# Optimization experiments

Hardware: AMD Instinct MI355X
Metric: run time of the kernel (lower is better)

## Reference

```python
import jax, jax.numpy as jnp
import numpy as np

N = 50000
E = 400000
IN_DIM = 64
HID = 64
HEADS = 4
LN_EPS = 1e-5


def _glorot(key, shape):
    fan_in, fan_out = shape[-1], shape[0] if len(shape) > 1 else shape[-1]
    lim = jnp.sqrt(6.0 / (fan_in + fan_out))
    return jax.random.uniform(key, shape, jnp.float32, -lim, lim)


def setup_inputs() -> dict:
    key = jax.random.key(0)
    ks = jax.random.split(key, 24)
    x = jax.random.normal(ks[0], (N, IN_DIM), jnp.float32)
    edge_index = jax.random.randint(ks[1], (2, E), 0, N, jnp.int64)
    role_ids = jax.random.randint(ks[2], (N,), 0, 2, jnp.int64)
    # GAT layer 1: in IN_DIM -> HEADS*HID, concat
    W1 = _glorot(ks[3], (HEADS * HID, IN_DIM))
    a1s = _glorot(ks[4], (HEADS, HID))
    a1d = _glorot(ks[5], (HEADS, HID))
    b1 = jnp.zeros((HEADS * HID,), jnp.float32)
    # GAT layer 2: HEADS*HID -> HEADS*HID, concat
    W2 = _glorot(ks[6], (HEADS * HID, HEADS * HID))
    a2s = _glorot(ks[7], (HEADS, HID))
    a2d = _glorot(ks[8], (HEADS, HID))
    b2 = jnp.zeros((HEADS * HID,), jnp.float32)
    # GAT layer 3: HEADS*HID -> HID, 1 head, no concat
    W3 = _glorot(ks[9], (HID, HEADS * HID))
    a3s = _glorot(ks[10], (1, HID))
    a3d = _glorot(ks[11], (1, HID))
    b3 = jnp.zeros((HID,), jnp.float32)
    ln1_w = jnp.ones((HEADS * HID,), jnp.float32); ln1_b = jnp.zeros((HEADS * HID,), jnp.float32)
    ln2_w = jnp.ones((HEADS * HID,), jnp.float32); ln2_b = jnp.zeros((HEADS * HID,), jnp.float32)
    ln3_w = jnp.ones((HID,), jnp.float32); ln3_b = jnp.zeros((HID,), jnp.float32)
    role_table = jax.random.normal(ks[12], (2, HID), jnp.float32)
    p1_w = _glorot(ks[13], (HID, 2 * HID)); p1_b = jnp.zeros((HID,), jnp.float32)
    p2_w = _glorot(ks[14], (HID, HID)); p2_b = jnp.zeros((HID,), jnp.float32)
    return dict(x=x, edge_index=edge_index, role_ids=role_ids,
                W1=W1, a1s=a1s, a1d=a1d, b1=b1,
                W2=W2, a2s=a2s, a2d=a2d, b2=b2,
                W3=W3, a3s=a3s, a3d=a3d, b3=b3,
                ln1_w=ln1_w, ln1_b=ln1_b, ln2_w=ln2_w, ln2_b=ln2_b,
                ln3_w=ln3_w, ln3_b=ln3_b,
                role_table=role_table, p1_w=p1_w, p1_b=p1_b, p2_w=p2_w, p2_b=p2_b)


def gat_conv(x, src, dst, W, a_src, a_dst, bias, heads, out_ch, concat):
    # x: [N, F_in]; src/dst: [E'] (self loops already appended)
    n = x.shape[0]
    h = (x @ W.T).reshape(n, heads, out_ch)              # [N,H,C]
    score_s = jnp.einsum('nhc,hc->nh', h, a_src)          # [N,H]
    score_d = jnp.einsum('nhc,hc->nh', h, a_dst)
    e = jax.nn.leaky_relu(score_s[src] + score_d[dst], 0.2)   # [E,H]
    m = jax.ops.segment_max(e, dst, num_segments=n)       # per-dst softmax
    e = jnp.exp(e - m[dst])
    s = jax.ops.segment_sum(e, dst, num_segments=n)
    alpha = e / (s[dst] + 1e-16)                          # [E,H]
    msg = h[src] * alpha[:, :, None]                      # [E,H,C]
    out = jax.ops.segment_sum(msg, dst, num_segments=n)   # [N,H,C]
    out = out.reshape(n, heads * out_ch) if concat else out.mean(axis=1)
    return out + bias


def layer_norm(x, w, b):
    mu = jnp.mean(x, axis=-1, keepdims=True)
    var = jnp.mean(jnp.square(x - mu), axis=-1, keepdims=True)
    return (x - mu) * jax.lax.rsqrt(var + LN_EPS) * w + b


def reference(x, edge_index, role_ids, W1, a1s, a1d, b1, W2, a2s, a2d, b2,
              W3, a3s, a3d, b3, ln1_w, ln1_b, ln2_w, ln2_b, ln3_w, ln3_b,
              role_table, p1_w, p1_b, p2_w, p2_b):
    n = x.shape[0]
    loop = jnp.arange(n, dtype=edge_index.dtype)
    src = jnp.concatenate([edge_index[0], loop])
    dst = jnp.concatenate([edge_index[1], loop])
    h = jax.nn.elu(gat_conv(x, src, dst, W1, a1s, a1d, b1, HEADS, HID, True))
    h = layer_norm(h, ln1_w, ln1_b)
    h = jax.nn.elu(gat_conv(h, src, dst, W2, a2s, a2d, b2, HEADS, HID, True))
    h = layer_norm(h, ln2_w, ln2_b)
    h = gat_conv(h, src, dst, W3, a3s, a3d, b3, 1, HID, False)
    h = layer_norm(h, ln3_w, ln3_b)
    role_emb = role_table[role_ids]                        # [N,HID]
    z = jnp.concatenate([h, role_emb], axis=-1)            # [N,2*HID]
    z = jax.nn.relu(z @ p1_w.T + p1_b)
    z = z @ p2_w.T + p2_b
    return z
```

## Files before the change

### kernel.cpp

```cpp
#include <hip/hip_runtime.h>
#include <math.h>


using short8 = __attribute__((ext_vector_type(8))) short;
using f32x4  = __attribute__((ext_vector_type(4))) float;

#define LOG2E 1.44269504088896340736f

__device__ __forceinline__ unsigned short f2bf(float f) {
    unsigned int u = __builtin_bit_cast(unsigned int, f);
    u += 0x7fffu + ((u >> 16) & 1u);
    return (unsigned short)(u >> 16);
}
__device__ __forceinline__ float bflo(unsigned int w) {
    return __builtin_bit_cast(float, w << 16);
}
__device__ __forceinline__ float bfhi(unsigned int w) {
    return __builtin_bit_cast(float, w & 0xffff0000u);
}
__device__ __forceinline__ float fexp2(float x) {
    return __builtin_amdgcn_exp2f(x);
}

__global__ void k_f2bf(const float* __restrict__ in, unsigned short* __restrict__ out,
                       int n) {
    int i = (blockIdx.x * 256 + threadIdx.x) * 4;
    if (i >= n) return;
    float4 v = *reinterpret_cast<const float4*>(in + i);
    ushort4 u;
    u.x = f2bf(v.x); u.y = f2bf(v.y); u.z = f2bf(v.z); u.w = f2bf(v.w);
    *reinterpret_cast<ushort4*>(out + i) = u;
}

__global__ void k_f2bf_w(const float* __restrict__ s0, unsigned short* __restrict__ d0, int n0,
                         const float* __restrict__ s1, unsigned short* __restrict__ d1, int n1,
                         const float* __restrict__ s2, unsigned short* __restrict__ d2, int n2,
                         const float* __restrict__ s3, unsigned short* __restrict__ d3, int n3,
                         const float* __restrict__ s4, unsigned short* __restrict__ d4, int n4) {
    int i = (blockIdx.x * 256 + threadIdx.x) * 4;
    const float* s; unsigned short* d; int off = i;
    if (off < n0) { s = s0; d = d0; }
    else if ((off -= n0) < n1) { s = s1; d = d1; }
    else if ((off -= n1) < n2) { s = s2; d = d2; }
    else if ((off -= n2) < n3) { s = s3; d = d3; }
    else if ((off -= n3) < n4) { s = s4; d = d4; }
    else return;
    float4 v = *reinterpret_cast<const float4*>(s + off);
    ushort4 u;
    u.x = f2bf(v.x); u.y = f2bf(v.y); u.z = f2bf(v.z); u.w = f2bf(v.w);
    *reinterpret_cast<ushort4*>(d + off) = u;
}

__global__ void k_count(const int* __restrict__ ei, int* __restrict__ deg,
                        int N, int E, int E2) {
    int i = blockIdx.x * 256 + threadIdx.x;
    if (i >= E2) return;
    int d = (i < E) ? ei[E + i] : (i - E);
    atomicAdd(&deg[d], 1);
}

__device__ __forceinline__ int blk_scan_incl(int v, int tid) {
    int lane = tid & 63, w = tid >> 6;
#pragma unroll
    for (int off = 1; off < 64; off <<= 1) {
        int u = __shfl_up(v, off);
        if (lane >= off) v += u;
    }
    __shared__ int wsum[4];
    if (lane == 63) wsum[w] = v;
    __syncthreads();
    int add = 0;
#pragma unroll
    for (int k = 0; k < 4; ++k)
        if (k < w) add += wsum[k];
    return v + add;
}

__global__ __launch_bounds__(256) void k_bsum(const int* __restrict__ deg,
                                              int* __restrict__ bsum, int N) {
    int i = blockIdx.x * 256 + threadIdx.x;
    int v = (i < N) ? deg[i] : 0;
#pragma unroll
    for (int off = 32; off; off >>= 1) v += __shfl_down(v, off);
    __shared__ int ws[4];
    if ((threadIdx.x & 63) == 0) ws[threadIdx.x >> 6] = v;
    __syncthreads();
    if (threadIdx.x == 0) bsum[blockIdx.x] = ws[0] + ws[1] + ws[2] + ws[3];
}

__global__ __launch_bounds__(256) void k_bscan(const int* __restrict__ bsum,
                                               int* __restrict__ boff, int nb) {
    int t = threadIdx.x;
    int v = (t < nb) ? bsum[t] : 0;
    int incl = blk_scan_incl(v, t);
    if (t < nb) boff[t] = incl - v;
}

__global__ __launch_bounds__(256) void k_scatter(const int* __restrict__ deg,
                                                 const int* __restrict__ boff,
                                                 int* __restrict__ row_ptr,
                                                 int* __restrict__ cursor,
                                                 int N, int E2) {
    int tid = threadIdx.x;
    int i = blockIdx.x * 256 + tid;
    int d = (i < N) ? deg[i] : 0;
    int incl = blk_scan_incl(d, tid);
    int ex = incl - d + boff[blockIdx.x];
    if (i < N) { row_ptr[i] = ex; cursor[i] = ex; }
    if (i == 0) row_ptr[N] = E2;
}

__global__ void k_fill(const int* __restrict__ ei, int* __restrict__ cursor,
                       int* __restrict__ edge_src, int N, int E, int E2) {
    int i = blockIdx.x * 256 + threadIdx.x;
    if (i >= E2) return;
    int s_, d_;
    if (i < E) { s_ = ei[i]; d_ = ei[E + i]; }
    else       { s_ = d_ = i - E; }
    int pos = atomicAdd(&cursor[d_], 1);
    edge_src[pos] = s_;
}

template <int K, bool RELU, bool BF16OUT, bool SCORES>
__global__ __launch_bounds__(256) void k_gmfma(const unsigned short* __restrict__ A,
                                               const unsigned short* __restrict__ Wb,
                                               const float* __restrict__ bias,
                                               void* __restrict__ Cv,
                                               float* __restrict__ sS,
                                               float* __restrict__ sD,
                                               const float* __restrict__ a_s,
                                               const float* __restrict__ a_d,
                                               int M, int NC, int Hs) {
    constexpr int NSTEP = K / 32;
    __shared__ unsigned short As[2][64 * 32];
    __shared__ unsigned short Bs[2][64 * 32];
    int tid = threadIdx.x;
    int lane = tid & 63, wid = tid >> 6;
    int wm = wid & 1, wn = wid >> 1;
    int fr = lane & 15, fq = lane >> 4;
    int bm = blockIdx.x * 64, bn = blockIdx.y * 64;

    int lrow = lane >> 2, lkq = (lane & 3) * 8;

    auto stage = [&](int buf, int k0) {
        int ra = wid * 16;
        int arow = min(bm + ra + lrow, M - 1);
        __builtin_amdgcn_global_load_lds(
            (const __attribute__((address_space(1))) unsigned int*)
                (A + (size_t)arow * K + k0 + lkq),
            (__attribute__((address_space(3))) unsigned int*)&As[buf][ra * 32],
            16, 0, 0);
        __builtin_amdgcn_global_load_lds(
            (const __attribute__((address_space(1))) unsigned int*)
                (Wb + (size_t)(bn + ra + lrow) * K + k0 + lkq),
            (__attribute__((address_space(3))) unsigned int*)&Bs[buf][ra * 32],
            16, 0, 0);
    };

    f32x4 acc[2][2];
#pragma unroll
    for (int mt = 0; mt < 2; ++mt)
#pragma unroll
        for (int nt = 0; nt < 2; ++nt) acc[mt][nt] = f32x4{0.f, 0.f, 0.f, 0.f};

    stage(0, 0);
    __syncthreads();
    int cur = 0;
    for (int t = 0; t < NSTEP; ++t) {
        if (t + 1 < NSTEP) stage(cur ^ 1, (t + 1) * 32);
        short8 af[2], bfr[2];
#pragma unroll
        for (int mt = 0; mt < 2; ++mt)
            af[mt] = *reinterpret_cast<const short8*>(
                &As[cur][(wm * 32 + mt * 16 + fr) * 32 + fq * 8]);
#pragma unroll
        for (int nt = 0; nt < 2; ++nt)
            bfr[nt] = *reinterpret_cast<const short8*>(
                &Bs[cur][(wn * 32 + nt * 16 + fr) * 32 + fq * 8]);
#pragma unroll
        for (int mt = 0; mt < 2; ++mt)
#pragma unroll
            for (int nt = 0; nt < 2; ++nt)
                acc[mt][nt] = __builtin_amdgcn_mfma_f32_16x16x32_bf16(
                    af[mt], bfr[nt], acc[mt][nt], 0, 0, 0);
        __syncthreads();
        cur ^= 1;
    }

#pragma unroll
    for (int nt = 0; nt < 2; ++nt) {
        int col = bn + wn * 32 + nt * 16 + fr;
        float bv = bias ? bias[col] : 0.f;
#pragma unroll
        for (int mt = 0; mt < 2; ++mt) {
#pragma unroll
            for (int j = 0; j < 4; ++j) {
                int row = bm + wm * 32 + mt * 16 + fq * 4 + j;
                if (row < M) {
                    float v = acc[mt][nt][j] + bv;
                    if (RELU) v = fmaxf(v, 0.f);
                    if constexpr (BF16OUT)
                        ((unsigned short*)Cv)[(size_t)row * NC + col] = f2bf(v);
                    else
                        ((float*)Cv)[(size_t)row * NC + col] = v;
                }
            }
        }
    }

    if constexpr (SCORES) {
        __shared__ float sps[2][64];
        __shared__ float spd[2][64];
        int head = blockIdx.y;
        float as_c[2], ad_c[2];
#pragma unroll
        for (int nt = 0; nt < 2; ++nt) {
            int cw = wn * 32 + nt * 16 + fr;
            as_c[nt] = a_s[head * 64 + cw];
            ad_c[nt] = a_d[head * 64 + cw];
        }
#pragma unroll
        for (int mt = 0; mt < 2; ++mt) {
#pragma unroll
            for (int j = 0; j < 4; ++j) {
                float ps = acc[mt][0][j] * as_c[0] + acc[mt][1][j] * as_c[1];
                float pd = acc[mt][0][j] * ad_c[0] + acc[mt][1][j] * ad_c[1];
#pragma unroll
                for (int off = 1; off < 16; off <<= 1) {
                    ps += __shfl_xor(ps, off);
                    pd += __shfl_xor(pd, off);
                }
                if (fr == 0) {
                    int rl = wm * 32 + mt * 16 + fq * 4 + j;
                    sps[wn][rl] = ps;
                    spd[wn][rl] = pd;
                }
            }
        }
        __syncthreads();
        if (tid < 64) {
            int row = bm + tid;
            if (row < M) {
                sS[(size_t)row * Hs + head] = (sps[0][tid] + sps[1][tid]) * LOG2E;
                sD[(size_t)row * Hs + head] = (spd[0][tid] + spd[1][tid]) * LOG2E;
            }
        }
    }
}

__global__ __launch_bounds__(256) void k_mlp(const unsigned short* __restrict__ catb,
                                             const unsigned short* __restrict__ p1wb,
                                             const float* __restrict__ p1b,
                                             const unsigned short* __restrict__ p2wb,
                                             const float* __restrict__ p2b,
                                             float* __restrict__ outp, int M) {
    __shared__ unsigned short As[2][64 * 32];
    __shared__ unsigned short Z1[64 * 72];
    int tid = threadIdx.x;
    int lane = tid & 63, wid = tid >> 6;
    int wm = wid & 1, wn = wid >> 1;
    int fr = lane & 15, fq = lane >> 4;
    int bm = blockIdx.x * 64;
    int lrow = lane >> 2, lkq = (lane & 3) * 8;

    auto stageA = [&](int buf, int k0) {
        int ra = wid * 16;
        int arow = min(bm + ra + lrow, M - 1);
        __builtin_amdgcn_global_load_lds(
            (const __attribute__((address_space(1))) unsigned int*)
                (catb + (size_t)arow * 128 + k0 + lkq),
            (__attribute__((address_space(3))) unsigned int*)&As[buf][ra * 32],
            16, 0, 0);
    };

    f32x4 acc[2][2];
#pragma unroll
    for (int mt = 0; mt < 2; ++mt)
#pragma unroll
        for (int nt = 0; nt < 2; ++nt) acc[mt][nt] = f32x4{0.f, 0.f, 0.f, 0.f};
    stageA(0, 0);
    __syncthreads();
    int cur = 0;
    for (int t = 0; t < 4; ++t) {
        if (t + 1 < 4) stageA(cur ^ 1, (t + 1) * 32);
        short8 af[2], bfr[2];
#pragma unroll
        for (int mt = 0; mt < 2; ++mt)
            af[mt] = *reinterpret_cast<const short8*>(
                &As[cur][(wm * 32 + mt * 16 + fr) * 32 + fq * 8]);
#pragma unroll
        for (int nt = 0; nt < 2; ++nt)
            bfr[nt] = *reinterpret_cast<const short8*>(
                p1wb + (size_t)(wn * 32 + nt * 16 + fr) * 128 + t * 32 + fq * 8);
#pragma unroll
        for (int mt = 0; mt < 2; ++mt)
#pragma unroll
            for (int nt = 0; nt < 2; ++nt)
                acc[mt][nt] = __builtin_amdgcn_mfma_f32_16x16x32_bf16(
                    af[mt], bfr[nt], acc[mt][nt], 0, 0, 0);
        __syncthreads();
        cur ^= 1;
    }
#pragma unroll
    for (int nt = 0; nt < 2; ++nt) {
        int col = wn * 32 + nt * 16 + fr;
        float bv = p1b[col];
#pragma unroll
        for (int mt = 0; mt < 2; ++mt) {
#pragma unroll
            for (int j = 0; j < 4; ++j) {
                int rl = wm * 32 + mt * 16 + fq * 4 + j;
                Z1[rl * 72 + col] = f2bf(fmaxf(acc[mt][nt][j] + bv, 0.f));
            }
        }
    }
    __syncthreads();

    f32x4 acc2[2][2];
#pragma unroll
    for (int mt = 0; mt < 2; ++mt)
#pragma unroll
        for (int nt = 0; nt < 2; ++nt) acc2[mt][nt] = f32x4{0.f, 0.f, 0.f, 0.f};
#pragma unroll
    for (int t = 0; t < 2; ++t) {
        short8 af[2], bfr[2];
#pragma unroll
        for (int mt = 0; mt < 2; ++mt)
            af[mt] = *reinterpret_cast<const short8*>(
                &Z1[(wm * 32 + mt * 16 + fr) * 72 + t * 32 + fq * 8]);
#pragma unroll
        for (int nt = 0; nt < 2; ++nt)
            bfr[nt] = *reinterpret_cast<const short8*>(
                p2wb + (size_t)(wn * 32 + nt * 16 + fr) * 64 + t * 32 + fq * 8);
#pragma unroll
        for (int mt = 0; mt < 2; ++mt)
#pragma unroll
            for (int nt = 0; nt < 2; ++nt)
                acc2[mt][nt] = __builtin_amdgcn_mfma_f32_16x16x32_bf16(
                    af[mt], bfr[nt], acc2[mt][nt], 0, 0, 0);
    }
#pragma unroll
    for (int nt = 0; nt < 2; ++nt) {
        int col = wn * 32 + nt * 16 + fr;
        float bv = p2b[col];
#pragma unroll
        for (int mt = 0; mt < 2; ++mt) {
#pragma unroll
            for (int j = 0; j < 4; ++j) {
                int row = bm + wm * 32 + mt * 16 + fq * 4 + j;
                if (row < M)
                    outp[(size_t)row * 64 + col] = acc2[mt][nt][j] + bv;
            }
        }
    }
}

template <int D, bool ELU, bool ROLE>
__global__ __launch_bounds__(256) void k_agg2(
        const unsigned short* __restrict__ hbf,
        const float* __restrict__ sS, const float* __restrict__ sD,
        const float* __restrict__ bias,
        const float* __restrict__ ln_w, const float* __restrict__ ln_b,
        const int* __restrict__ row_ptr, const int* __restrict__ edge_src,
        const int* __restrict__ role_ids, const float* __restrict__ role_table,
        unsigned short* __restrict__ out, int N, int ostride) {
    constexpr int H = D / 64;
    constexpr int CPT = 8;
    constexpr int TPN = D / CPT;
    constexpr int NPB = 256 / TPN;
    int tid = threadIdx.x;
    int n = blockIdx.x * NPB + tid / TPN;
    int t = tid % TPN;
    if (n >= N) return;
    int rs = row_ptr[n], re = row_ptr[n + 1];

    int c0 = CPT * t;
    int hh = c0 >> 6;
    float sdn = sD[(size_t)n * H + hh];

    float s = 0.f;
    float a[CPT] = {};
#pragma unroll 2
    for (int i = rs; i < re; ++i) {
        int src = edge_src[i];
        float e = sS[(size_t)src * H + hh] + sdn;
        e = e > 0.f ? e : 0.2f * e;
        float p = fexp2(e);
        s += p;
        uint4 u = *reinterpret_cast<const uint4*>(hbf + (size_t)src * D + c0);
        a[0] += p * bflo(u.x); a[1] += p * bfhi(u.x);
        a[2] += p * bflo(u.y); a[3] += p * bfhi(u.y);
        a[4] += p * bflo(u.z); a[5] += p * bfhi(u.z);
        a[6] += p * bflo(u.w); a[7] += p * bfhi(u.w);
    }
    float inv = 1.f / (s + 1e-16f);

    float v[CPT];
    float sum = 0.f, sq = 0.f;
#pragma unroll
    for (int j = 0; j < CPT; ++j) {
        float w = a[j] * inv + bias[c0 + j];
        if (ELU) w = w > 0.f ? w : (__expf(w) - 1.f);
        v[j] = w;
        sum += w; sq += w * w;
    }
#pragma unroll
    for (int off = 1; off < TPN; off <<= 1) {
        sum += __shfl_xor(sum, off);
        sq += __shfl_xor(sq, off);
    }
    float mu = sum / D;
    float var = fmaxf(sq / D - mu * mu, 0.f);
    float rstd = rsqrtf(var + 1e-5f);
    unsigned int w01, w23, w45, w67;
    {
        float y0 = (v[0] - mu) * rstd * ln_w[c0 + 0] + ln_b[c0 + 0];
        float y1 = (v[1] - mu) * rstd * ln_w[c0 + 1] + ln_b[c0 + 1];
        w01 = (unsigned int)f2bf(y0) | ((unsigned int)f2bf(y1) << 16);
        float y2 = (v[2] - mu) * rstd * ln_w[c0 + 2] + ln_b[c0 + 2];
        float y3 = (v[3] - mu) * rstd * ln_w[c0 + 3] + ln_b[c0 + 3];
        w23 = (unsigned int)f2bf(y2) | ((unsigned int)f2bf(y3) << 16);
        float y4 = (v[4] - mu) * rstd * ln_w[c0 + 4] + ln_b[c0 + 4];
        float y5 = (v[5] - mu) * rstd * ln_w[c0 + 5] + ln_b[c0 + 5];
        w45 = (unsigned int)f2bf(y4) | ((unsigned int)f2bf(y5) << 16);
        float y6 = (v[6] - mu) * rstd * ln_w[c0 + 6] + ln_b[c0 + 6];
        float y7 = (v[7] - mu) * rstd * ln_w[c0 + 7] + ln_b[c0 + 7];
        w67 = (unsigned int)f2bf(y6) | ((unsigned int)f2bf(y7) << 16);
    }
    uint4 o;
    o.x = w01; o.y = w23; o.z = w45; o.w = w67;
    *reinterpret_cast<uint4*>(out + (size_t)n * ostride + c0) = o;

    if constexpr (ROLE) {
        int rid = role_ids[n];
        float4 r0 = *reinterpret_cast<const float4*>(role_table + rid * 64 + c0);
        float4 r1 = *reinterpret_cast<const float4*>(role_table + rid * 64 + c0 + 4);
        uint4 ro;
        ro.x = (unsigned int)f2bf(r0.x) | ((unsigned int)f2bf(r0.y) << 16);
        ro.y = (unsigned int)f2bf(r0.z) | ((unsigned int)f2bf(r0.w) << 16);
        ro.z = (unsigned int)f2bf(r1.x) | ((unsigned int)f2bf(r1.y) << 16);
        ro.w = (unsigned int)f2bf(r1.z) | ((unsigned int)f2bf(r1.w) << 16);
        *reinterpret_cast<uint4*>(out + (size_t)n * ostride + 64 + c0) = ro;
    }
}

extern "C" void kernel_launch(void* const* d_in, const int* in_sizes, int n_in,
                              void* d_out, int out_size, void* d_ws, size_t ws_size,
                              hipStream_t stream) {
    const float* x        = (const float*)d_in[0];
    const int*   ei       = (const int*)d_in[1];
    const int*   role_ids = (const int*)d_in[2];
    const float* W1  = (const float*)d_in[3];
    const float* a1s = (const float*)d_in[4];
    const float* a1d = (const float*)d_in[5];
    const float* b1  = (const float*)d_in[6];
    const float* W2  = (const float*)d_in[7];
    const float* a2s = (const float*)d_in[8];
    const float* a2d = (const float*)d_in[9];
    const float* b2  = (const float*)d_in[10];
    const float* W3  = (const float*)d_in[11];
    const float* a3s = (const float*)d_in[12];
    const float* a3d = (const float*)d_in[13];
    const float* b3  = (const float*)d_in[14];
    const float* ln1w = (const float*)d_in[15];
    const float* ln1b = (const float*)d_in[16];
    const float* ln2w = (const float*)d_in[17];
    const float* ln2b = (const float*)d_in[18];
    const float* ln3w = (const float*)d_in[19];
    const float* ln3b = (const float*)d_in[20];
    const float* role_table = (const float*)d_in[21];
    const float* p1w = (const float*)d_in[22];
    const float* p1b = (const float*)d_in[23];
    const float* p2w = (const float*)d_in[24];
    const float* p2b = (const float*)d_in[25];

    const int N = in_sizes[0] / 64;
    const int E = in_sizes[1] / 2;
    const int E2 = E + N;

    char* p = (char*)d_ws;
    auto carve = [&](size_t bytes) -> char* {
        char* r = p;
        p += (bytes + 255) & ~(size_t)255;
        return r;
    };
    int* deg      = (int*)carve((size_t)N * 4);
    int* row_ptr  = (int*)carve((size_t)(N + 1) * 4);
    int* cursor   = (int*)carve((size_t)N * 4);
    int* edge_src = (int*)carve((size_t)E2 * 4);
    int* bsum     = (int*)carve((size_t)1024 * 4);
    int* boff     = (int*)carve((size_t)1024 * 4);
    float* sS     = (float*)carve((size_t)N * 4 * 4);
    float* sD     = (float*)carve((size_t)N * 4 * 4);
    unsigned short* hbf  = (unsigned short*)carve((size_t)N * 256 * 2);
    unsigned short* hlnb = (unsigned short*)carve((size_t)N * 256 * 2);
    unsigned short* catb = (unsigned short*)carve((size_t)N * 128 * 2);
    unsigned short* xb   = (unsigned short*)carve((size_t)N * 64 * 2);
    unsigned short* W1b  = (unsigned short*)carve((size_t)256 * 64 * 2);
    unsigned short* W2b  = (unsigned short*)carve((size_t)256 * 256 * 2);
    unsigned short* W3b  = (unsigned short*)carve((size_t)64 * 256 * 2);
    unsigned short* p1wb = (unsigned short*)carve((size_t)64 * 128 * 2);
    unsigned short* p2wb = (unsigned short*)carve((size_t)64 * 64 * 2);

    k_f2bf<<<(N * 64 / 4 + 255) / 256, 256, 0, stream>>>(x, xb, N * 64);
    {
        int n0 = 256 * 64, n1 = 256 * 256, n2 = 64 * 256, n3 = 64 * 128, n4 = 64 * 64;
        int tot = n0 + n1 + n2 + n3 + n4;
        k_f2bf_w<<<(tot / 4 + 255) / 256, 256, 0, stream>>>(
            W1, W1b, n0, W2, W2b, n1, W3, W3b, n2, p1w, p1wb, n3, p2w, p2wb, n4);
    }

    hipMemsetAsync(deg, 0, (size_t)N * 4, stream);
    int eb = (E2 + 255) / 256;
    int nb = (N + 255) / 256;
    k_count<<<eb, 256, 0, stream>>>(ei, deg, N, E, E2);
    k_bsum<<<nb, 256, 0, stream>>>(deg, bsum, N);
    k_bscan<<<1, 256, 0, stream>>>(bsum, boff, nb);
    k_scatter<<<nb, 256, 0, stream>>>(deg, boff, row_ptr, cursor, N, E2);
    k_fill<<<eb, 256, 0, stream>>>(ei, cursor, edge_src, N, E, E2);

    int mb = (N + 63) / 64;

    k_gmfma<64, false, true, true><<<dim3(mb, 4), 256, 0, stream>>>(
        xb, W1b, nullptr, hbf, sS, sD, a1s, a1d, N, 256, 4);
    k_agg2<256, true, false><<<(N + 7) / 8, 256, 0, stream>>>(
        hbf, sS, sD, b1, ln1w, ln1b, row_ptr, edge_src,
        nullptr, nullptr, hlnb, N, 256);

    k_gmfma<256, false, true, true><<<dim3(mb, 4), 256, 0, stream>>>(
        hlnb, W2b, nullptr, hbf, sS, sD, a2s, a2d, N, 256, 4);
    k_agg2<256, true, false><<<(N + 7) / 8, 256, 0, stream>>>(
        hbf, sS, sD, b2, ln2w, ln2b, row_ptr, edge_src,
        nullptr, nullptr, hlnb, N, 256);

    k_gmfma<256, false, true, true><<<dim3(mb, 1), 256, 0, stream>>>(
        hlnb, W3b, nullptr, hbf, sS, sD, a3s, a3d, N, 64, 1);
    k_agg2<64, false, true><<<(N + 31) / 32, 256, 0, stream>>>(
        hbf, sS, sD, b3, ln3w, ln3b, row_ptr, edge_src,
        role_ids, role_table, catb, N, 128);

    k_mlp<<<mb, 256, 0, stream>>>(catb, p1wb, p1b, p2wb, p2b, (float*)d_out, N);
}
```

Before: 236.3 us.

## Process aggregation nodes in degree-sorted order to balance per-wave work

Adds a stable counting sort of nodes by in-degree (histogram per block, global scan, per-block rank) to build a permutation. The three aggregation kernels then pick their node through this permutation, so nodes sharing a wavefront have similar edge counts and fewer lanes sit idle waiting on long neighbour lists. The cost is three extra small kernels plus an indirection, and the scattered node order may hurt output-write and row_ptr locality.

```diff
diff --git a/kernel.cpp b/kernel.cpp
--- a/kernel.cpp
+++ b/kernel.cpp
@@ -119,6 +119,50 @@
     else       { s_ = d_ = i - E; }
     int pos = atomicAdd(&cursor[d_], 1);
     edge_src[pos] = s_;
+}
+
+__global__ __launch_bounds__(256) void k_hist2(const int* __restrict__ deg,
+                                               int* __restrict__ hist2,
+                                               int N, int nb) {
+    __shared__ int lh[64];
+    int tid = threadIdx.x;
+    if (tid < 64) lh[tid] = 0;
+    __syncthreads();
+    int i = blockIdx.x * 256 + tid;
+    if (i < N) atomicAdd(&lh[min(deg[i], 63)], 1);
+    __syncthreads();
+    if (tid < 64) hist2[tid * nb + blockIdx.x] = lh[tid];
+}
+
+__global__ __launch_bounds__(256) void k_scan2(int* __restrict__ hist2, int total) {
+    int tid = threadIdx.x;
+    int chunk = (total + 255) / 256;
+    int st = tid * chunk, en = min(total, st + chunk);
+    int s = 0;
+    for (int i = st; i < en; ++i) s += hist2[i];
+    int incl = blk_scan_incl(s, tid);
+    int run = incl - s;
+    for (int i = st; i < en; ++i) {
+        int v = hist2[i];
+        hist2[i] = run;
+        run += v;
+    }
+}
+
+__global__ __launch_bounds__(256) void k_order2(const int* __restrict__ deg,
+                                                const int* __restrict__ seg,
+                                                int* __restrict__ order,
+                                                int N, int nb) {
+    __shared__ unsigned char sbin[256];
+    int tid = threadIdx.x;
+    int i = blockIdx.x * 256 + tid;
+    int bin = (i < N) ? min(deg[i], 63) : 255;
+    sbin[tid] = (unsigned char)bin;
+    __syncthreads();
+    if (i >= N) return;
+    int rank = 0;
+    for (int j = 0; j < tid; ++j) rank += (sbin[j] == (unsigned char)bin);
+    order[seg[bin * nb + blockIdx.x] + rank] = i;
 }
 
 template <int K, bool RELU, bool BF16OUT, bool SCORES>
@@ -362,6 +406,7 @@
         const float* __restrict__ bias,
         const float* __restrict__ ln_w, const float* __restrict__ ln_b,
         const int* __restrict__ row_ptr, const int* __restrict__ edge_src,
+        const int* __restrict__ order,
         const int* __restrict__ role_ids, const float* __restrict__ role_table,
         unsigned short* __restrict__ out, int N, int ostride) {
     constexpr int H = D / 64;
@@ -369,9 +414,10 @@
     constexpr int TPN = D / CPT;
     constexpr int NPB = 256 / TPN;
     int tid = threadIdx.x;
-    int n = blockIdx.x * NPB + tid / TPN;
+    int g = blockIdx.x * NPB + tid / TPN;
     int t = tid % TPN;
-    if (n >= N) return;
+    if (g >= N) return;
+    int n = order[g];
     int rs = row_ptr[n], re = row_ptr[n + 1];
 
     int c0 = CPT * t;
@@ -484,12 +530,15 @@
         p += (bytes + 255) & ~(size_t)255;
         return r;
     };
+    int nb = (N + 255) / 256;
     int* deg      = (int*)carve((size_t)N * 4);
     int* row_ptr  = (int*)carve((size_t)(N + 1) * 4);
     int* cursor   = (int*)carve((size_t)N * 4);
     int* edge_src = (int*)carve((size_t)E2 * 4);
     int* bsum     = (int*)carve((size_t)1024 * 4);
     int* boff     = (int*)carve((size_t)1024 * 4);
+    int* hist2    = (int*)carve((size_t)64 * nb * 4);
+    int* order    = (int*)carve((size_t)N * 4);
     float* sS     = (float*)carve((size_t)N * 4 * 4);
     float* sD     = (float*)carve((size_t)N * 4 * 4);
     unsigned short* hbf  = (unsigned short*)carve((size_t)N * 256 * 2);
@@ -512,31 +561,33 @@
 
     hipMemsetAsync(deg, 0, (size_t)N * 4, stream);
     int eb = (E2 + 255) / 256;
-    int nb = (N + 255) / 256;
     k_count<<<eb, 256, 0, stream>>>(ei, deg, N, E, E2);
     k_bsum<<<nb, 256, 0, stream>>>(deg, bsum, N);
     k_bscan<<<1, 256, 0, stream>>>(bsum, boff, nb);
     k_scatter<<<nb, 256, 0, stream>>>(deg, boff, row_ptr, cursor, N, E2);
     k_fill<<<eb, 256, 0, stream>>>(ei, cursor, edge_src, N, E, E2);
+    k_hist2<<<nb, 256, 0, stream>>>(deg, hist2, N, nb);
+    k_scan2<<<1, 256, 0, stream>>>(hist2, 64 * nb);
+    k_order2<<<nb, 256, 0, stream>>>(deg, hist2, order, N, nb);
 
     int mb = (N + 63) / 64;
 
     k_gmfma<64, false, true, true><<<dim3(mb, 4), 256, 0, stream>>>(
         xb, W1b, nullptr, hbf, sS, sD, a1s, a1d, N, 256, 4);
     k_agg2<256, true, false><<<(N + 7) / 8, 256, 0, stream>>>(
-        hbf, sS, sD, b1, ln1w, ln1b, row_ptr, edge_src,
+        hbf, sS, sD, b1, ln1w, ln1b, row_ptr, edge_src, order,
         nullptr, nullptr, hlnb, N, 256);
 
     k_gmfma<256, false, true, true><<<dim3(mb, 4), 256, 0, stream>>>(
         hlnb, W2b, nullptr, hbf, sS, sD, a2s, a2d, N, 256, 4);
     k_agg2<256, true, false><<<(N + 7) / 8, 256, 0, stream>>>(
-        hbf, sS, sD, b2, ln2w, ln2b, row_ptr, edge_src,
+        hbf, sS, sD, b2, ln2w, ln2b, row_ptr, edge_src, order,
         nullptr, nullptr, hlnb, N, 256);
 
     k_gmfma<256, false, true, true><<<dim3(mb, 1), 256, 0, stream>>>(
         hlnb, W3b, nullptr, hbf, sS, sD, a3s, a3d, N, 64, 1);
     k_agg2<64, false, true><<<(N + 31) / 32, 256, 0, stream>>>(
-        hbf, sS, sD, b3, ln3w, ln3b, row_ptr, edge_src,
+        hbf, sS, sD, b3, ln3w, ln3b, row_ptr, edge_src, order,
         role_ids, role_table, catb, N, 128);
 
     k_mlp<<<mb, 256, 0, stream>>>(catb, p1wb, p1b, p2wb, p2b, (float*)d_out, N);
```

Result: slower. 268.2 us (+13.5%).
